# Kernel tuning notes

Measured on AMD Instinct MI355X. Metric: run time of the kernel, lower is better.

The kernel has to match this reference:

```python
import math
import jax, jax.numpy as jnp
import numpy as np

D_HEAD = 64
KS = 7
EPS = 1e-6


def _rope_freqs(d_head, n_heads):
    # AxialRoPE buffer: exp(linspace(log(pi), log(10*pi), nh*dim//4+1)[:-1]).view(dim//4, nh).T
    dim = d_head // 2
    n = n_heads * dim // 4
    f = np.exp(np.linspace(math.log(math.pi), math.log(10.0 * math.pi), n + 1)[:-1]).astype(np.float32)
    return jnp.asarray(f.reshape(dim // 4, n_heads).T)  # [nh, dim//4]


def setup_inputs() -> dict:
    key = jax.random.key(0)
    ks = jax.random.split(key, 6)
    B, C, T, H, W = 1, 512, 4, 32, 32
    cond_features = 256
    nh = C // D_HEAD
    x = jax.random.normal(ks[0], (B, C, T, H, W), dtype=jnp.float32)
    pos = jax.random.uniform(ks[1], (B, H, W, 2), dtype=jnp.float32)
    cond = jax.random.normal(ks[2], (B, cond_features), dtype=jnp.float32)
    # zero-init layers in the original (norm.linear, out_proj) get small random weights
    # here so the reference exercises nontrivial math/gradients.
    norm_w = jax.random.normal(ks[3], (cond_features, C), dtype=jnp.float32) * 0.02
    qkv_w = jax.random.normal(ks[4], (C, 3 * C), dtype=jnp.float32) * (1.0 / math.sqrt(C))
    out_w = jax.random.normal(ks[5], (C, C), dtype=jnp.float32) * (1.0 / math.sqrt(C))
    scale = jnp.full((nh,), 10.0, dtype=jnp.float32)
    return {"x": x, "pos": pos, "cond": cond, "norm_w": norm_w, "qkv_w": qkv_w,
            "scale": scale, "out_w": out_w}


def reference(x, pos, cond, norm_w, qkv_w, scale, out_w):
    B, C, T, H, W = x.shape
    nh = C // D_HEAD
    N = B * T
    skip = x

    # b c t h w -> (b t) h w c
    xr = jnp.transpose(x, (0, 2, 3, 4, 1)).reshape(N, H, W, C)
    condr = jnp.repeat(cond, T, axis=0)  # (b t) c, b-major

    # AdaRMSNorm: scale = linear(cond) + 1, applied with rms normalization
    s = condr @ norm_w + 1.0  # [N, C]
    mean_sq = jnp.mean(xr * xr, axis=-1, keepdims=True)
    xn = xr * (s[:, None, None, :] * jax.lax.rsqrt(mean_sq + EPS))

    qkv = (xn @ qkv_w).reshape(N, H, W, 3, nh, D_HEAD)
    q, k, v = qkv[:, :, :, 0], qkv[:, :, :, 1], qkv[:, :, :, 2]  # [N,H,W,nh,e]

    # cosine-sim scaling per head
    sqrt_scale = jnp.sqrt(scale)[:, None]  # [nh,1]
    q = q * (sqrt_scale * jax.lax.rsqrt(jnp.sum(q * q, -1, keepdims=True) + EPS))
    k = k * (sqrt_scale * jax.lax.rsqrt(jnp.sum(k * k, -1, keepdims=True) + EPS))

    # axial RoPE
    freqs = _rope_freqs(D_HEAD, nh)  # [nh, e//8]
    theta = jnp.concatenate([pos[..., None, 0:1] * freqs,
                             pos[..., None, 1:2] * freqs], axis=-1)  # [B,H,W,nh,e//4]
    theta = jnp.repeat(theta, T, axis=0)  # [N,H,W,nh,d]
    d = theta.shape[-1]
    cos_t, sin_t = jnp.cos(theta), jnp.sin(theta)

    def rope(t):
        x1, x2, x3 = t[..., :d], t[..., d:2 * d], t[..., 2 * d:]
        return jnp.concatenate([x1 * cos_t - x2 * sin_t,
                                x2 * cos_t + x1 * sin_t, x3], axis=-1)

    q, k = rope(q), rope(k)

    # neighborhood attention (NATTEN na2d semantics: window clamped to image border)
    r = KS // 2
    ih = jnp.clip(jnp.arange(H) - r, 0, H - KS)[:, None] + jnp.arange(KS)  # [H,KS]
    iw = jnp.clip(jnp.arange(W) - r, 0, W - KS)[:, None] + jnp.arange(KS)  # [W,KS]

    def windows(t):  # [N,H,W,nh,e] -> [N,H,W,KS*KS,nh,e]
        g = t[:, ih[:, :, None, None], iw[None, None, :, :]]  # [N,H,KS,W,KS,nh,e]
        return jnp.transpose(g, (0, 1, 3, 2, 4, 5, 6)).reshape(N, H, W, KS * KS, nh, D_HEAD)

    kw, vw = windows(k), windows(v)
    logits = jnp.einsum('nhwce,nhwkce->nhwck', q, kw)  # scale=1.0 in na2d call
    attn = jax.nn.softmax(logits, axis=-1)
    o = jnp.einsum('nhwck,nhwkce->nhwce', attn, vw).reshape(N, H, W, C)

    y = o @ out_w  # dropout=0.0
    y = jnp.transpose(y.reshape(B, T, H, W, C), (0, 4, 1, 2, 3))
    return y + skip
```

## Files before the change

### kernel.cpp

```cpp
#include <hip/hip_runtime.h>
#include <hip/hip_bf16.h>

typedef __hip_bfloat16 bf16;
#define F32(b) __bfloat162float(b)
#define B16(f) __float2bfloat16(f)

typedef __attribute__((ext_vector_type(8))) short short8;
typedef __attribute__((ext_vector_type(4))) float f32x4;

#define C_DIM 512
#define P_DIM 4096

__global__ __launch_bounds__(256) void k_prep(const float* __restrict__ cond,
                                              const float* __restrict__ norm_w,
                                              const float* __restrict__ x,
                                              const float* __restrict__ qkv_w,
                                              const float* __restrict__ out_w,
                                              float* __restrict__ s,
                                              float* __restrict__ rms_part,
                                              bf16* __restrict__ qkvT,
                                              bf16* __restrict__ outT){
  __shared__ float sh[64 * 65];
  int bid = blockIdx.x;
  int tid = threadIdx.x;
  if (bid < 16){
    int c_l = tid & 31, fo = tid >> 5;
    int c = bid * 32 + c_l;
    float acc = 0.f;
    for (int f = fo * 32; f < fo * 32 + 32; ++f)
      acc = fmaf(cond[f], norm_w[f * 512 + c], acc);
    sh[fo * 33 + c_l] = acc;
    __syncthreads();
    if (tid < 32){
      float a = 0.f;
#pragma unroll
      for (int i = 0; i < 8; ++i) a += sh[i * 33 + tid];
      s[bid * 32 + tid] = a + 1.0f;
    }
  } else if (bid < 528){
    int b = bid - 16;
    int bp = b & 63, bc = b >> 6;
    int co = tid >> 6, pl = tid & 63;
    int p = bp * 64 + pl;
    float acc = 0.f;
    for (int c = bc * 64 + co; c < bc * 64 + 64; c += 4){
      float v = x[c * P_DIM + p];
      acc = fmaf(v, v, acc);
    }
    sh[co * 64 + pl] = acc;
    __syncthreads();
    if (tid < 64)
      rms_part[bc * P_DIM + bp * 64 + tid] = sh[tid] + sh[64 + tid] + sh[128 + tid] + sh[192 + tid];
  } else {
    int b = bid - 528;
    const float* src; bf16* dst; int NW, n0, c0;
    if (b < 192){ src = qkv_w; dst = qkvT; NW = 1536; n0 = (b % 24) * 64; c0 = (b / 24) * 64; }
    else { int bb = b - 192; src = out_w; dst = outT; NW = 512; n0 = (bb & 7) * 64; c0 = (bb >> 3) * 64; }
    int grp = tid >> 6, lane = tid & 63;
    for (int i = grp; i < 64; i += 4)
      sh[i * 65 + lane] = src[(c0 + i) * NW + n0 + lane];
    __syncthreads();
    for (int j = grp; j < 64; j += 4)
      dst[(n0 + j) * 512 + c0 + lane] = B16(sh[lane * 65 + j]);
  }
}

__global__ __launch_bounds__(256) void k_xnt(const float* __restrict__ x,
                                             const float* __restrict__ s,
                                             const float* __restrict__ rms_part,
                                             bf16* __restrict__ xn){
  __shared__ float tile[64][65];
  int bp = blockIdx.x & 63, bc = blockIdx.x >> 6;
  int p0 = bp * 64, c0 = bc * 64;
  int grp = threadIdx.x >> 6, lane = threadIdx.x & 63;
  for (int i = grp; i < 64; i += 4)
    tile[i][lane] = x[(c0 + i) * P_DIM + p0 + lane] * s[c0 + i];
  __syncthreads();
  for (int j = grp; j < 64; j += 4){
    float ss = 0.f;
#pragma unroll
    for (int i = 0; i < 8; ++i) ss += rms_part[i * P_DIM + p0 + j];
    float rv = rsqrtf(ss * (1.0f / 512.0f) + 1e-6f);
    xn[(size_t)(p0 + j) * 512 + c0 + lane] = B16(tile[lane][j] * rv);
  }
}

#define AS 72
__global__ __launch_bounds__(256) void k_gemm_qkv(const bf16* __restrict__ Ab,
                                                  const bf16* __restrict__ BTb,
                                                  const float* __restrict__ scale,
                                                  const float* __restrict__ pos,
                                                  bf16* __restrict__ qkv_bf){
  __shared__ unsigned short a_t[128 * AS];
  __shared__ unsigned short b_t[64 * AS];
  const unsigned short* A  = (const unsigned short*)Ab;
  const unsigned short* BT = (const unsigned short*)BTb;
  int m0 = blockIdx.x * 128;
  int by = blockIdx.y;
  int n0 = by * 64;
  int tid = threadIdx.x;
  int w = tid >> 6, l = tid & 63, g = l >> 4, cb = l & 15;

  f32x4 acc[2][4];
#pragma unroll
  for (int mi = 0; mi < 2; ++mi)
#pragma unroll
    for (int nj = 0; nj < 4; ++nj)
#pragma unroll
      for (int r = 0; r < 4; ++r) acc[mi][nj][r] = 0.f;

  for (int kk = 0; kk < 512; kk += 64){
#pragma unroll
    for (int i = 0; i < 4; ++i){
      int sid = tid + i * 256;
      int row = sid >> 3, seg = sid & 7;
      *(uint4*)&a_t[row * AS + seg * 8] = *(const uint4*)&A[(size_t)(m0 + row) * 512 + kk + seg * 8];
    }
#pragma unroll
    for (int i = 0; i < 2; ++i){
      int sid = tid + i * 256;
      int row = sid >> 3, seg = sid & 7;
      *(uint4*)&b_t[row * AS + seg * 8] = *(const uint4*)&BT[(size_t)(n0 + row) * 512 + kk + seg * 8];
    }
    __syncthreads();
#pragma unroll
    for (int kc = 0; kc < 2; ++kc){
      short8 af[2];
#pragma unroll
      for (int mi = 0; mi < 2; ++mi)
        af[mi] = *(const short8*)&a_t[(w * 32 + mi * 16 + cb) * AS + kc * 32 + g * 8];
#pragma unroll
      for (int nj = 0; nj < 4; ++nj){
        short8 bfr = *(const short8*)&b_t[(nj * 16 + cb) * AS + kc * 32 + g * 8];
#pragma unroll
        for (int mi = 0; mi < 2; ++mi)
          acc[mi][nj] = __builtin_amdgcn_mfma_f32_16x16x32_bf16(af[mi], bfr, acc[mi][nj], 0, 0, 0);
      }
    }
    __syncthreads();
  }

  if (by < 16){
    int head = by & 7;
    float sqs = sqrtf(scale[head]);
    int axis = cb >> 3, i = cb & 7;
    const float LOG_PI = 1.1447298858494002f;
    const float LOG10F = 2.302585092994046f;
    float f = __expf(LOG_PI + (float)(i * 8 + head) * (LOG10F / 64.0f));
#pragma unroll
    for (int mi = 0; mi < 2; ++mi)
#pragma unroll
      for (int r = 0; r < 4; ++r){
        float ss = 0.f;
#pragma unroll
        for (int nj = 0; nj < 4; ++nj) ss = fmaf(acc[mi][nj][r], acc[mi][nj][r], ss);
#pragma unroll
        for (int off = 1; off < 16; off <<= 1) ss += __shfl_xor(ss, off, 64);
        float fac = sqs * rsqrtf(ss + 1e-6f);
        int rowg = m0 + w * 32 + mi * 16 + g * 4 + r;
        float th = pos[(rowg & 1023) * 2 + axis] * f;
        float ct = __cosf(th), st = __sinf(th);
        float v0 = acc[mi][0][r] * fac, v1 = acc[mi][1][r] * fac;
        acc[mi][0][r] = v0 * ct - v1 * st;
        acc[mi][1][r] = v1 * ct + v0 * st;
        acc[mi][2][r] *= fac;
        acc[mi][3][r] *= fac;
      }
  }

#pragma unroll
  for (int mi = 0; mi < 2; ++mi)
#pragma unroll
    for (int nj = 0; nj < 4; ++nj){
      int col = n0 + nj * 16 + cb;
#pragma unroll
      for (int r = 0; r < 4; ++r){
        int rowg = m0 + w * 32 + mi * 16 + g * 4 + r;
        qkv_bf[(size_t)rowg * 1536 + col] = B16(acc[mi][nj][r]);
      }
    }
}

#define KL_S 80
#define VT_S 232
#define PP_S 232
__global__ __launch_bounds__(256) void k_attn(const bf16* __restrict__ qkv_bfp,
                                              bf16* __restrict__ o_bf){
  __shared__ unsigned short kp[208 * KL_S];
  __shared__ unsigned short vT[64 * VT_S];
  const unsigned short* qkv = (const unsigned short*)qkv_bfp;

  int bid = blockIdx.x;
  int head = bid & 7;
  int patch = bid >> 3;
  int t = patch >> 4;
  int ph = (patch >> 2) & 3, pw = patch & 3;
  int h0 = ph * 8, w0 = pw * 8;
  int rs = min(max(h0 - 3, 0), 18);
  int cs = min(max(w0 - 3, 0), 18);
  int tbase = t << 10;
  int tid = threadIdx.x;
  int cp = tid & 31, pxg = tid >> 5;

  for (int i = 0; i < 26; ++i){
    int px = i * 8 + pxg;
    unsigned val = 0;
    if (px < 196){
      int rr = px / 14, cc = px - rr * 14;
      size_t pn = (size_t)(tbase + (rs + rr) * 32 + (cs + cc));
      val = *(const unsigned*)&qkv[pn * 1536 + 512 + head * 64 + cp * 2];
    }
    *(unsigned*)&kp[px * KL_S + cp * 2] = val;
  }
  for (int i = 0; i < 14; ++i){
    int pp = i * 8 + pxg;
    int px0 = 2 * pp, px1 = px0 + 1;
    unsigned v0 = 0, v1 = 0;
    if (px0 < 196){
      int rr = px0 / 14, cc = px0 - rr * 14;
      size_t pn = (size_t)(tbase + (rs + rr) * 32 + (cs + cc));
      v0 = *(const unsigned*)&qkv[pn * 1536 + 1024 + head * 64 + cp * 2];
    }
    if (px1 < 196){
      int rr = px1 / 14, cc = px1 - rr * 14;
      size_t pn = (size_t)(tbase + (rs + rr) * 32 + (cs + cc));
      v1 = *(const unsigned*)&qkv[pn * 1536 + 1024 + head * 64 + cp * 2];
    }
    unsigned lo = (v0 & 0xffffu) | (v1 << 16);
    unsigned hi = (v0 >> 16) | (v1 & 0xffff0000u);
    *(unsigned*)&vT[(2 * cp) * VT_S + 2 * pp] = lo;
    *(unsigned*)&vT[(2 * cp + 1) * VT_S + 2 * pp] = hi;
  }

  int w = tid >> 6, l = tid & 63;
  int g = l >> 4, cb = l & 15;

  int q_a = w * 16 + cb;
  size_t abase = (size_t)(tbase + (h0 + (q_a >> 3)) * 32 + (w0 + (q_a & 7))) * 1536 + head * 64;
  short8 qa0 = *(const short8*)&qkv[abase + g * 8];
  short8 qa1 = *(const short8*)&qkv[abase + 32 + g * 8];

  __syncthreads();

  f32x4 acc[13];
#pragma unroll
  for (int nt = 0; nt < 13; ++nt)
#pragma unroll
    for (int r = 0; r < 4; ++r) acc[nt][r] = 0.f;
#pragma unroll
  for (int nt = 0; nt < 13; ++nt){
    short8 kb0 = *(const short8*)&kp[(nt * 16 + cb) * KL_S + g * 8];
    short8 kb1 = *(const short8*)&kp[(nt * 16 + cb) * KL_S + 32 + g * 8];
    acc[nt] = __builtin_amdgcn_mfma_f32_16x16x32_bf16(qa0, kb0, acc[nt], 0, 0, 0);
    acc[nt] = __builtin_amdgcn_mfma_f32_16x16x32_bf16(qa1, kb1, acc[nt], 0, 0, 0);
  }
  __syncthreads();

  int wr0[4], wc0[4];
#pragma unroll
  for (int r = 0; r < 4; ++r){
    int q_l = w * 16 + g * 4 + r;
    int hq = h0 + (q_l >> 3), wq = w0 + (q_l & 7);
    wr0[r] = min(max(hq - 3, 0), 25) - rs;
    wc0[r] = min(max(wq - 3, 0), 25) - cs;
  }
  float mx[4] = {-1e30f, -1e30f, -1e30f, -1e30f};
#pragma unroll
  for (int nt = 0; nt < 13; ++nt){
    int kg = nt * 16 + cb;
    int kr = kg / 14, kc = kg - kr * 14;
    bool kvalid = kg < 196;
#pragma unroll
    for (int r = 0; r < 4; ++r){
      bool v = kvalid && ((unsigned)(kr - wr0[r]) < 7u) && ((unsigned)(kc - wc0[r]) < 7u);
      float lg = v ? acc[nt][r] : -1e30f;
      acc[nt][r] = lg;
      mx[r] = fmaxf(mx[r], lg);
    }
  }
#pragma unroll
  for (int off = 1; off < 16; off <<= 1)
#pragma unroll
    for (int r = 0; r < 4; ++r) mx[r] = fmaxf(mx[r], __shfl_xor(mx[r], off, 64));
  float sm[4] = {0.f, 0.f, 0.f, 0.f};
#pragma unroll
  for (int nt = 0; nt < 13; ++nt)
#pragma unroll
    for (int r = 0; r < 4; ++r){
      float e = __expf(acc[nt][r] - mx[r]);
      acc[nt][r] = e;
      sm[r] += e;
    }
#pragma unroll
  for (int off = 1; off < 16; off <<= 1)
#pragma unroll
    for (int r = 0; r < 4; ++r) sm[r] += __shfl_xor(sm[r], off, 64);
  float inv[4];
#pragma unroll
  for (int r = 0; r < 4; ++r) inv[r] = 1.0f / sm[r];

#pragma unroll
  for (int nt = 0; nt < 13; ++nt)
#pragma unroll
    for (int r = 0; r < 4; ++r)
      *reinterpret_cast<bf16*>(&kp[(w * 16 + g * 4 + r) * PP_S + nt * 16 + cb]) = B16(acc[nt][r] * inv[r]);
#pragma unroll
  for (int r = 0; r < 4; ++r)
    kp[(w * 16 + g * 4 + r) * PP_S + 208 + cb] = 0;
  __syncthreads();

  f32x4 acc2[4];
#pragma unroll
  for (int ct = 0; ct < 4; ++ct)
#pragma unroll
    for (int r = 0; r < 4; ++r) acc2[ct][r] = 0.f;
#pragma unroll
  for (int kt = 0; kt < 7; ++kt){
    short8 pa = *(const short8*)&kp[(w * 16 + cb) * PP_S + kt * 32 + g * 8];
#pragma unroll
    for (int ct = 0; ct < 4; ++ct){
      short8 vb = *(const short8*)&vT[(ct * 16 + cb) * VT_S + kt * 32 + g * 8];
      acc2[ct] = __builtin_amdgcn_mfma_f32_16x16x32_bf16(pa, vb, acc2[ct], 0, 0, 0);
    }
  }
#pragma unroll
  for (int ct = 0; ct < 4; ++ct)
#pragma unroll
    for (int r = 0; r < 4; ++r){
      int q_l = w * 16 + g * 4 + r;
      int p = tbase + (h0 + (q_l >> 3)) * 32 + (w0 + (q_l & 7));
      o_bf[(size_t)p * 512 + head * 64 + ct * 16 + cb] = B16(acc2[ct][r]);
    }
}

__global__ __launch_bounds__(256) void k_gemm_out(const bf16* __restrict__ Ab,
                                                  const bf16* __restrict__ BTb,
                                                  const float* __restrict__ xres,
                                                  float* __restrict__ out){
  __shared__ unsigned short a_t[128 * AS];
  __shared__ unsigned short b_t[64 * AS];
  __shared__ float tile[64][65];
  const unsigned short* A  = (const unsigned short*)Ab;
  const unsigned short* BT = (const unsigned short*)BTb;
  int m0 = blockIdx.x * 128;
  int n0 = blockIdx.y * 64;
  int tid = threadIdx.x;
  int w = tid >> 6, l = tid & 63, g = l >> 4, cb = l & 15;

  f32x4 acc[2][4];
#pragma unroll
  for (int mi = 0; mi < 2; ++mi)
#pragma unroll
    for (int nj = 0; nj < 4; ++nj)
#pragma unroll
      for (int r = 0; r < 4; ++r) acc[mi][nj][r] = 0.f;

  for (int kk = 0; kk < 512; kk += 64){
#pragma unroll
    for (int i = 0; i < 4; ++i){
      int sid = tid + i * 256;
      int row = sid >> 3, seg = sid & 7;
      *(uint4*)&a_t[row * AS + seg * 8] = *(const uint4*)&A[(size_t)(m0 + row) * 512 + kk + seg * 8];
    }
#pragma unroll
    for (int i = 0; i < 2; ++i){
      int sid = tid + i * 256;
      int row = sid >> 3, seg = sid & 7;
      *(uint4*)&b_t[row * AS + seg * 8] = *(const uint4*)&BT[(size_t)(n0 + row) * 512 + kk + seg * 8];
    }
    __syncthreads();
#pragma unroll
    for (int kc = 0; kc < 2; ++kc){
      short8 af[2];
#pragma unroll
      for (int mi = 0; mi < 2; ++mi)
        af[mi] = *(const short8*)&a_t[(w * 32 + mi * 16 + cb) * AS + kc * 32 + g * 8];
#pragma unroll
      for (int nj = 0; nj < 4; ++nj){
        short8 bfr = *(const short8*)&b_t[(nj * 16 + cb) * AS + kc * 32 + g * 8];
#pragma unroll
        for (int mi = 0; mi < 2; ++mi)
          acc[mi][nj] = __builtin_amdgcn_mfma_f32_16x16x32_bf16(af[mi], bfr, acc[mi][nj], 0, 0, 0);
      }
    }
    __syncthreads();
  }
  int grp = tid >> 6, lane = tid & 63;
#pragma unroll
  for (int hh = 0; hh < 2; ++hh){
    __syncthreads();
    if ((w >> 1) == hh){
#pragma unroll
      for (int mi = 0; mi < 2; ++mi)
#pragma unroll
        for (int nj = 0; nj < 4; ++nj)
#pragma unroll
          for (int r = 0; r < 4; ++r)
            tile[(w & 1) * 32 + mi * 16 + g * 4 + r][nj * 16 + cb] = acc[mi][nj][r];
    }
    __syncthreads();
    for (int j2 = grp; j2 < 64; j2 += 4){
      int c = n0 + j2;
      int p = m0 + hh * 64 + lane;
      out[(size_t)c * P_DIM + p] = tile[lane][j2] + xres[(size_t)c * P_DIM + p];
    }
  }
}

extern "C" void kernel_launch(void* const* d_in, const int* in_sizes, int n_in,
                              void* d_out, int out_size, void* d_ws, size_t ws_size,
                              hipStream_t stream){
  const float* x      = (const float*)d_in[0];
  const float* pos    = (const float*)d_in[1];
  const float* cond   = (const float*)d_in[2];
  const float* norm_w = (const float*)d_in[3];
  const float* qkv_w  = (const float*)d_in[4];
  const float* scale  = (const float*)d_in[5];
  const float* out_w  = (const float*)d_in[6];
  float* out = (float*)d_out;

  char* wp = (char*)d_ws;
  auto alloc = [&](size_t bytes) -> char* {
    char* r = wp;
    wp += (bytes + 255) & ~((size_t)255);
    return r;
  };
  float* s_f      = (float*)alloc(512 * 4);
  float* rms_part = (float*)alloc(8 * 4096 * 4);
  bf16*  xn       = (bf16*) alloc((size_t)4096 * 512 * 2);
  bf16*  qkvT     = (bf16*) alloc((size_t)1536 * 512 * 2);
  bf16*  outT     = (bf16*) alloc((size_t)512 * 512 * 2);
  bf16*  qkv_bf   = (bf16*) alloc((size_t)4096 * 1536 * 2);
  bf16*  o_bf     = (bf16*) alloc((size_t)4096 * 512 * 2);

  k_prep    <<<784,         256, 0, stream>>>(cond, norm_w, x, qkv_w, out_w,
                                              s_f, rms_part, qkvT, outT);
  k_xnt     <<<512,         256, 0, stream>>>(x, s_f, rms_part, xn);
  k_gemm_qkv<<<dim3(32,24), 256, 0, stream>>>(xn, qkvT, scale, pos, qkv_bf);
  k_attn    <<<512,         256, 0, stream>>>(qkv_bf, o_bf);
  k_gemm_out<<<dim3(32,8),  256, 0, stream>>>(o_bf, outT, x, out);
}
```

Before: 130.5 us.

## Fuse prep and normalization kernels into one launch with redundant per-block reductions

```diff
diff --git a/kernel.cpp b/kernel.cpp
--- a/kernel.cpp
+++ b/kernel.cpp
@@ -2,90 +2,81 @@
 #include <hip/hip_bf16.h>
 
 typedef __hip_bfloat16 bf16;
-#define F32(b) __bfloat162float(b)
 #define B16(f) __float2bfloat16(f)
 
 typedef __attribute__((ext_vector_type(8))) short short8;
 typedef __attribute__((ext_vector_type(4))) float f32x4;
 
-#define C_DIM 512
 #define P_DIM 4096
-
-__global__ __launch_bounds__(256) void k_prep(const float* __restrict__ cond,
-                                              const float* __restrict__ norm_w,
-                                              const float* __restrict__ x,
-                                              const float* __restrict__ qkv_w,
-                                              const float* __restrict__ out_w,
-                                              float* __restrict__ s,
-                                              float* __restrict__ rms_part,
-                                              bf16* __restrict__ qkvT,
-                                              bf16* __restrict__ outT){
+#define AS   72
+
+__global__ __launch_bounds__(256) void k_pre(const float* __restrict__ x,
+                                             const float* __restrict__ cond,
+                                             const float* __restrict__ norm_w,
+                                             const float* __restrict__ qkv_w,
+                                             const float* __restrict__ out_w,
+                                             bf16* __restrict__ qkvT,
+                                             bf16* __restrict__ outT,
+                                             bf16* __restrict__ xn){
   __shared__ float sh[64 * 65];
+  __shared__ float s_red[4][64];
+  __shared__ float s_sh[64];
+  __shared__ float ssv[64];
   int bid = blockIdx.x;
   int tid = threadIdx.x;
-  if (bid < 16){
-    int c_l = tid & 31, fo = tid >> 5;
-    int c = bid * 32 + c_l;
-    float acc = 0.f;
-    for (int f = fo * 32; f < fo * 32 + 32; ++f)
-      acc = fmaf(cond[f], norm_w[f * 512 + c], acc);
-    sh[fo * 33 + c_l] = acc;
-    __syncthreads();
-    if (tid < 32){
-      float a = 0.f;
-#pragma unroll
-      for (int i = 0; i < 8; ++i) a += sh[i * 33 + tid];
-      s[bid * 32 + tid] = a + 1.0f;
-    }
-  } else if (bid < 528){
-    int b = bid - 16;
-    int bp = b & 63, bc = b >> 6;
-    int co = tid >> 6, pl = tid & 63;
-    int p = bp * 64 + pl;
-    float acc = 0.f;
-    for (int c = bc * 64 + co; c < bc * 64 + 64; c += 4){
-      float v = x[c * P_DIM + p];
-      acc = fmaf(v, v, acc);
-    }
-    sh[co * 64 + pl] = acc;
-    __syncthreads();
-    if (tid < 64)
-      rms_part[bc * P_DIM + bp * 64 + tid] = sh[tid] + sh[64 + tid] + sh[128 + tid] + sh[192 + tid];
-  } else {
-    int b = bid - 528;
+  int grp = tid >> 6, lane = tid & 63;
+
+  if (bid < 256){
+    int b = bid;
     const float* src; bf16* dst; int NW, n0, c0;
     if (b < 192){ src = qkv_w; dst = qkvT; NW = 1536; n0 = (b % 24) * 64; c0 = (b / 24) * 64; }
     else { int bb = b - 192; src = out_w; dst = outT; NW = 512; n0 = (bb & 7) * 64; c0 = (bb >> 3) * 64; }
-    int grp = tid >> 6, lane = tid & 63;
     for (int i = grp; i < 64; i += 4)
       sh[i * 65 + lane] = src[(c0 + i) * NW + n0 + lane];
     __syncthreads();
     for (int j = grp; j < 64; j += 4)
       dst[(n0 + j) * 512 + c0 + lane] = B16(sh[lane * 65 + j]);
-  }
-}
-
-__global__ __launch_bounds__(256) void k_xnt(const float* __restrict__ x,
-                                             const float* __restrict__ s,
-                                             const float* __restrict__ rms_part,
-                                             bf16* __restrict__ xn){
-  __shared__ float tile[64][65];
-  int bp = blockIdx.x & 63, bc = blockIdx.x >> 6;
+    return;
+  }
+
+  int b = bid - 256;
+  int bp = b & 63, bc = b >> 6;
   int p0 = bp * 64, c0 = bc * 64;
-  int grp = threadIdx.x >> 6, lane = threadIdx.x & 63;
+
+  {
+    float acc = 0.f;
+    for (int f = grp * 64; f < grp * 64 + 64; ++f)
+      acc = fmaf(cond[f], norm_w[f * 512 + c0 + lane], acc);
+    s_red[grp][lane] = acc;
+  }
+  {
+    float acc = 0.f;
+    for (int c = grp * 128; c < grp * 128 + 128; ++c){
+      float v = x[c * P_DIM + p0 + lane];
+      acc = fmaf(v, v, acc);
+    }
+    __syncthreads();
+    if (grp == 0) ssv[lane] = acc;
+    __syncthreads();
+    if (grp == 1) ssv[lane] += acc;
+    __syncthreads();
+    if (grp == 2) ssv[lane] += acc;
+    __syncthreads();
+    if (grp == 3) ssv[lane] += acc;
+    if (tid < 64)
+      s_sh[tid] = s_red[0][tid] + s_red[1][tid] + s_red[2][tid] + s_red[3][tid] + 1.0f;
+  }
+  __syncthreads();
+
   for (int i = grp; i < 64; i += 4)
-    tile[i][lane] = x[(c0 + i) * P_DIM + p0 + lane] * s[c0 + i];
+    sh[i * 65 + lane] = x[(c0 + i) * P_DIM + p0 + lane] * s_sh[i];
   __syncthreads();
   for (int j = grp; j < 64; j += 4){
-    float ss = 0.f;
-#pragma unroll
-    for (int i = 0; i < 8; ++i) ss += rms_part[i * P_DIM + p0 + j];
-    float rv = rsqrtf(ss * (1.0f / 512.0f) + 1e-6f);
-    xn[(size_t)(p0 + j) * 512 + c0 + lane] = B16(tile[lane][j] * rv);
+    float rv = rsqrtf(ssv[j] * (1.0f / 512.0f) + 1e-6f);
+    xn[(size_t)(p0 + j) * 512 + c0 + lane] = B16(sh[lane * 65 + j] * rv);
   }
 }
 
-#define AS 72
 __global__ __launch_bounds__(256) void k_gemm_qkv(const bf16* __restrict__ Ab,
                                                   const bf16* __restrict__ BTb,
                                                   const float* __restrict__ scale,
@@ -143,10 +134,10 @@
   if (by < 16){
     int head = by & 7;
     float sqs = sqrtf(scale[head]);
-    int axis = cb >> 3, i = cb & 7;
+    int axis = cb >> 3, fi = cb & 7;
     const float LOG_PI = 1.1447298858494002f;
     const float LOG10F = 2.302585092994046f;
-    float f = __expf(LOG_PI + (float)(i * 8 + head) * (LOG10F / 64.0f));
+    float f = __expf(LOG_PI + (float)(fi * 8 + head) * (LOG10F / 64.0f));
 #pragma unroll
     for (int mi = 0; mi < 2; ++mi)
 #pragma unroll
@@ -425,17 +416,14 @@
     wp += (bytes + 255) & ~((size_t)255);
     return r;
   };
-  float* s_f      = (float*)alloc(512 * 4);
-  float* rms_part = (float*)alloc(8 * 4096 * 4);
   bf16*  xn       = (bf16*) alloc((size_t)4096 * 512 * 2);
   bf16*  qkvT     = (bf16*) alloc((size_t)1536 * 512 * 2);
   bf16*  outT     = (bf16*) alloc((size_t)512 * 512 * 2);
   bf16*  qkv_bf   = (bf16*) alloc((size_t)4096 * 1536 * 2);
   bf16*  o_bf     = (bf16*) alloc((size_t)4096 * 512 * 2);
 
-  k_prep    <<<784,         256, 0, stream>>>(cond, norm_w, x, qkv_w, out_w,
-                                              s_f, rms_part, qkvT, outT);
-  k_xnt     <<<512,         256, 0, stream>>>(x, s_f, rms_part, xn);
+  k_pre     <<<768,         256, 0, stream>>>(x, cond, norm_w, qkv_w, out_w,
+                                              qkvT, outT, xn);
   k_gemm_qkv<<<dim3(32,24), 256, 0, stream>>>(xn, qkvT, scale, pos, qkv_bf);
   k_attn    <<<512,         256, 0, stream>>>(qkv_bf, o_bf);
   k_gemm_out<<<dim3(32,8),  256, 0, stream>>>(o_bf, outT, x, out);
```

New measurement: 166.2 us. +27.4%, slower.
